# Optimization experiments

Measured on AMD Instinct MI355X. Metric: run time of the kernel, lower is better.

## Reference

```python
import jax, jax.numpy as jnp
import numpy as np

N, E = 50000, 800000
F_IN, F_EDGE = 64, 16
HEADS, C_HEAD = 4, 32
HC = HEADS * C_HEAD  # 128 = hidden_node_channels
MLP_IN = F_IN + HC   # 192
MLP0, MLP1 = 128, 128
NEG_SLOPE = 0.2


def leaky_relu(x):
    return jnp.where(x >= 0, x, NEG_SLOPE * x)


def layer_norm(x, g, b, eps=1e-5):
    mu = jnp.mean(x, axis=-1, keepdims=True)
    var = jnp.mean(jnp.square(x - mu), axis=-1, keepdims=True)
    return (x - mu) * jax.lax.rsqrt(var + eps) * g + b


def setup_inputs() -> dict:
    key = jax.random.key(0)
    ks = jax.random.split(key, 24)
    s = 0.05
    inp = {
        "node_features": jax.random.normal(ks[0], (N, F_IN), jnp.float32),
        "edge_features": jax.random.normal(ks[1], (E, F_EDGE), jnp.float32),
        "edge_index": jax.random.randint(ks[2], (2, E), 0, N, jnp.int32),
        # GATv2Conv params (share_weights=False, bias=True, edge_dim=16)
        "W_l": jax.random.normal(ks[3], (F_IN, HC), jnp.float32) * s,
        "b_l": jax.random.normal(ks[4], (HC,), jnp.float32) * s,
        "W_r": jax.random.normal(ks[5], (F_IN, HC), jnp.float32) * s,
        "b_r": jax.random.normal(ks[6], (HC,), jnp.float32) * s,
        "W_e": jax.random.normal(ks[7], (F_EDGE, HC), jnp.float32) * s,
        "att": jax.random.normal(ks[8], (HEADS, C_HEAD), jnp.float32) * s,
        "gat_bias": jax.random.normal(ks[9], (HC,), jnp.float32) * s,
        # residual_connection: Linear(64->128) + LayerNorm
        "res_W": jax.random.normal(ks[10], (F_IN, MLP1), jnp.float32) * s,
        "res_b": jax.random.normal(ks[11], (MLP1,), jnp.float32) * s,
        "res_g": 1.0 + jax.random.normal(ks[12], (MLP1,), jnp.float32) * s,
        "res_beta": jax.random.normal(ks[13], (MLP1,), jnp.float32) * s,
        # upd MLP: two ffn_blocks (Linear -> LayerNorm -> ReLU)
        "W0": jax.random.normal(ks[14], (MLP_IN, MLP0), jnp.float32) * s,
        "b0": jax.random.normal(ks[15], (MLP0,), jnp.float32) * s,
        "g0": 1.0 + jax.random.normal(ks[16], (MLP0,), jnp.float32) * s,
        "beta0": jax.random.normal(ks[17], (MLP0,), jnp.float32) * s,
        "W1": jax.random.normal(ks[18], (MLP0, MLP1), jnp.float32) * s,
        "b1": jax.random.normal(ks[19], (MLP1,), jnp.float32) * s,
        "g1": 1.0 + jax.random.normal(ks[20], (MLP1,), jnp.float32) * s,
        "beta1": jax.random.normal(ks[21], (MLP1,), jnp.float32) * s,
    }
    return inp


def reference(node_features, edge_features, edge_index,
              W_l, b_l, W_r, b_r, W_e, att, gat_bias,
              res_W, res_b, res_g, res_beta,
              W0, b0, g0, beta0, W1, b1, g1, beta1):
    src, dst = edge_index[0], edge_index[1]

    # ---- GATv2Conv ----
    x_l = (node_features @ W_l + b_l).reshape(N, HEADS, C_HEAD)  # source transform
    x_r = (node_features @ W_r + b_r).reshape(N, HEADS, C_HEAD)  # target transform
    e = (edge_features @ W_e).reshape(E, HEADS, C_HEAD)

    x_j = x_l[src]                      # [E,H,C] messages
    m = x_j + x_r[dst] + e              # [E,H,C]
    logits = jnp.sum(leaky_relu(m) * att, axis=-1)  # [E,H]

    # segment softmax over incoming edges of each destination node
    mx = jax.ops.segment_max(logits, dst, num_segments=N)      # [N,H]
    ex = jnp.exp(logits - mx[dst])                             # [E,H]
    den = jax.ops.segment_sum(ex, dst, num_segments=N)         # [N,H]
    alpha = ex / den[dst]                                      # [E,H]

    agg = jax.ops.segment_sum(alpha[..., None] * x_j, dst, num_segments=N)
    gat_out = agg.reshape(N, HC) + gat_bias                    # [N,128]

    # ---- residual concat-MLP ----
    identity = layer_norm(node_features @ res_W + res_b, res_g, res_beta)
    h = jnp.concatenate([node_features, gat_out], axis=-1)     # [N,192]
    h = jax.nn.relu(layer_norm(h @ W0 + b0, g0, beta0))
    h = jax.nn.relu(layer_norm(h @ W1 + b1, g1, beta1))
    return identity + h
```

## Files before the change

### kernel.cpp

```cpp
#include <hip/hip_runtime.h>

#define NN 50000
#define NE 800000
#define NB 196
#define K1B 782

typedef __attribute__((ext_vector_type(8))) short bf16x8;
typedef __attribute__((ext_vector_type(4))) float f32x4;
typedef __attribute__((ext_vector_type(2))) _Float16 h2f;

__device__ __forceinline__ int rfl(int v) { return __builtin_amdgcn_readfirstlane(v); }

__device__ __forceinline__ unsigned short bfb(float x) {
    union { float f; unsigned u; } v; v.f = x;
    unsigned r = v.u + 0x7FFFu + ((v.u >> 16) & 1u);
    return (unsigned short)(r >> 16);
}
__device__ __forceinline__ unsigned pkbf(float lo, float hi) {
    return ((unsigned)bfb(hi) << 16) | (unsigned)bfb(lo);
}
__device__ __forceinline__ float bf2f(unsigned short s) {
    union { unsigned u; float f; } v; v.u = ((unsigned)s) << 16; return v.f;
}
__device__ __forceinline__ unsigned pkh2(float a, float b) {
    union { h2f h; unsigned u; } x;
    x.h.x = (_Float16)a; x.h.y = (_Float16)b;
    return x.u;
}
__device__ __forceinline__ float fdot2u(unsigned a, unsigned b, float c) {
    union { unsigned u; h2f h; } ua, ub; ua.u = a; ub.u = b;
    return __builtin_amdgcn_fdot2(ua.h, ub.h, c, false);
}

__device__ __forceinline__ float dpp_reduce16(float p) {
    int t;
    t = __builtin_amdgcn_update_dpp(0, __float_as_int(p), 0xB1, 0xF, 0xF, false);
    p += __int_as_float(t);
    t = __builtin_amdgcn_update_dpp(0, __float_as_int(p), 0x4E, 0xF, 0xF, false);
    p += __int_as_float(t);
    t = __builtin_amdgcn_update_dpp(0, __float_as_int(p), 0x124, 0xF, 0xF, false);
    p += __int_as_float(t);
    t = __builtin_amdgcn_update_dpp(0, __float_as_int(p), 0x128, 0xF, 0xF, false);
    p += __int_as_float(t);
    return p;
}

__device__ __forceinline__ float exp2_hw(float x) {
    float r;
    asm("v_exp_f32 %0, %1" : "=v"(r) : "v"(x));
    return r;
}

__global__ __launch_bounds__(256) void k0_prep(
    const float* __restrict__ W_l, const float* __restrict__ W_r,
    const float* __restrict__ res_W, const float* __restrict__ W0,
    const float* __restrict__ W1, const float* __restrict__ W_e,
    unsigned short* __restrict__ Wtl, unsigned short* __restrict__ Wtr,
    unsigned short* __restrict__ Wtres, unsigned short* __restrict__ Wt0,
    unsigned short* __restrict__ Wt1,
    unsigned* __restrict__ Wep,
    int* __restrict__ deg, int* __restrict__ row_start)
{
    const int t0 = blockIdx.x * 256 + threadIdx.x;
    if (t0 < 24576) { int n = t0 / 192, k = t0 - n * 192; Wt0[t0] = bfb(W0[k * 128 + n]); }
    if (t0 < 16384) { int n = t0 >> 7, k = t0 & 127; Wt1[t0] = bfb(W1[k * 128 + n]); }
    if (t0 < 8192) {
        int n = t0 >> 6, k = t0 & 63;
        Wtl[t0]   = bfb(W_l[k * 128 + n]);
        Wtr[t0]   = bfb(W_r[k * 128 + n]);
        Wtres[t0] = bfb(res_W[k * 128 + n]);
    }
    if (t0 < 1024) {
        int c = t0 >> 3, j = t0 & 7;
        Wep[t0] = pkh2(W_e[(2 * j) * 128 + c], W_e[(2 * j + 1) * 128 + c]);
    }
    if (t0 < NN) deg[t0] = 0;
    if (t0 == 0) row_start[NN] = NE;
}

__global__ __launch_bounds__(256, 4) void ka_nodes_degree(
    const float* __restrict__ nf,
    const unsigned short* __restrict__ Wtl, const float* __restrict__ b_l,
    const unsigned short* __restrict__ Wtr, const float* __restrict__ b_r,
    const unsigned short* __restrict__ Wtres, const float* __restrict__ res_b,
    const float* __restrict__ res_g, const float* __restrict__ res_beta,
    unsigned* __restrict__ xlp, unsigned* __restrict__ xrp,
    unsigned* __restrict__ identp,
    const int* __restrict__ eidx, int* __restrict__ deg, int* __restrict__ rank,
    const float* __restrict__ ef, unsigned* __restrict__ efp)
{
    if (blockIdx.x >= K1B) {
        int e = (blockIdx.x - K1B) * 256 + threadIdx.x;
        if (e < NE) {
            rank[e] = atomicAdd(deg + eidx[NE + e], 1);
            const float4* er = (const float4*)(ef + (size_t)e * 16);
            float4 v0 = er[0], v1 = er[1], v2 = er[2], v3 = er[3];
            uint4 o0, o1;
            o0.x = pkh2(v0.x, v0.y); o0.y = pkh2(v0.z, v0.w);
            o0.z = pkh2(v1.x, v1.y); o0.w = pkh2(v1.z, v1.w);
            o1.x = pkh2(v2.x, v2.y); o1.y = pkh2(v2.z, v2.w);
            o1.z = pkh2(v3.x, v3.y); o1.w = pkh2(v3.z, v3.w);
            *(uint4*)(efp + (size_t)e * 8)     = o0;
            *(uint4*)(efp + (size_t)e * 8 + 4) = o1;
        }
        return;
    }
    __shared__ __align__(16) unsigned As32[64 * 36];
    const int tid = threadIdx.x;
    const int node0 = blockIdx.x * 64;

    for (int i = tid; i < 64 * 32; i += 256) {
        int n = i >> 5, c2 = i & 31;
        int gn = node0 + n;
        float2 v = make_float2(0.f, 0.f);
        if (gn < NN) v = *(const float2*)(nf + gn * 64 + 2 * c2);
        As32[n * 36 + c2] = pkbf(v.x, v.y);
    }
    __syncthreads();

    const int lane = tid & 63, w = tid >> 6;
    const int c = lane & 15, ko = lane >> 4;
    const unsigned short* As = (const unsigned short*)As32;
    bf16x8 a0 = *(const bf16x8*)(As + (w * 16 + c) * 72 + 0 * 32 + ko * 8);
    bf16x8 a1 = *(const bf16x8*)(As + (w * 16 + c) * 72 + 1 * 32 + ko * 8);
    const int lrow0 = node0 + w * 16 + 4 * ko;

    #pragma unroll
    for (int p = 0; p < 3; ++p) {
        const unsigned short* Wt = (p == 0) ? Wtl : (p == 1) ? Wtr : Wtres;
        f32x4 acc[8];
        #pragma unroll
        for (int nt = 0; nt < 8; ++nt) acc[nt] = f32x4{0.f, 0.f, 0.f, 0.f};
        #pragma unroll
        for (int nt = 0; nt < 8; ++nt) {
            bf16x8 bf0 = *(const bf16x8*)(Wt + (nt * 16 + c) * 64 + 0 * 32 + ko * 8);
            acc[nt] = __builtin_amdgcn_mfma_f32_16x16x32_bf16(a0, bf0, acc[nt], 0, 0, 0);
            bf16x8 bf1 = *(const bf16x8*)(Wt + (nt * 16 + c) * 64 + 1 * 32 + ko * 8);
            acc[nt] = __builtin_amdgcn_mfma_f32_16x16x32_bf16(a1, bf1, acc[nt], 0, 0, 0);
        }
        if (p < 2) {
            const float* bias = (p == 0) ? b_l : b_r;
            unsigned* outp = (p == 0) ? xlp : xrp;
            float bv[8];
            #pragma unroll
            for (int nt = 0; nt < 8; ++nt) bv[nt] = bias[nt * 16 + c];
            #pragma unroll
            for (int reg = 0; reg < 4; ++reg) {
                int row = lrow0 + reg;
                #pragma unroll
                for (int nt = 0; nt < 8; ++nt) {
                    float v = acc[nt][reg] + bv[nt];
                    float v2 = __shfl_xor(v, 1, 64);
                    if (row < NN && (lane & 1) == 0)
                        outp[row * 64 + nt * 8 + (c >> 1)] = pkh2(v, v2);
                }
            }
        } else {
            float bv[8], gv[8], tv[8];
            #pragma unroll
            for (int nt = 0; nt < 8; ++nt) {
                bv[nt] = res_b[nt * 16 + c];
                gv[nt] = res_g[nt * 16 + c];
                tv[nt] = res_beta[nt * 16 + c];
            }
            #pragma unroll
            for (int reg = 0; reg < 4; ++reg) {
                float sum = 0.f, sq = 0.f, hv[8];
                #pragma unroll
                for (int nt = 0; nt < 8; ++nt) {
                    float v = acc[nt][reg] + bv[nt];
                    hv[nt] = v; sum += v; sq += v * v;
                }
                #pragma unroll
                for (int m = 1; m <= 8; m <<= 1) {
                    sum += __shfl_xor(sum, m, 64);
                    sq  += __shfl_xor(sq, m, 64);
                }
                float mean = sum * (1.f / 128.f);
                float inv  = rsqrtf(sq * (1.f / 128.f) - mean * mean + 1e-5f);
                int row = lrow0 + reg;
                #pragma unroll
                for (int nt = 0; nt < 8; ++nt) {
                    float v = (hv[nt] - mean) * inv * gv[nt] + tv[nt];
                    float v2 = __shfl_xor(v, 1, 64);
                    if (row < NN && (lane & 1) == 0)
                        identp[row * 64 + nt * 8 + (c >> 1)] = pkbf(v, v2);
                }
            }
        }
    }
}

__global__ __launch_bounds__(256) void k3a_blocksum(
    const int* __restrict__ deg, int* __restrict__ bsum)
{
    __shared__ int ws[4];
    int i = blockIdx.x * 256 + threadIdx.x;
    int v = (i < NN) ? deg[i] : 0;
    #pragma unroll
    for (int m = 32; m >= 1; m >>= 1) v += __shfl_xor(v, m, 64);
    if ((threadIdx.x & 63) == 0) ws[threadIdx.x >> 6] = v;
    __syncthreads();
    if (threadIdx.x == 0) bsum[blockIdx.x] = ws[0] + ws[1] + ws[2] + ws[3];
}

__global__ __launch_bounds__(256) void k3c_apply(
    const int* __restrict__ deg, const int* __restrict__ bsum,
    int* __restrict__ row_start)
{
    __shared__ int wsum[4];
    __shared__ int roff[4];
    const int tid = threadIdx.x, lane = tid & 63, wid = tid >> 6;
    int bv = (tid < blockIdx.x) ? bsum[tid] : 0;
    #pragma unroll
    for (int m = 32; m >= 1; m >>= 1) bv += __shfl_xor(bv, m, 64);
    if (lane == 0) roff[wid] = bv;

    int i = blockIdx.x * 256 + tid;
    int v = (i < NN) ? deg[i] : 0;
    int sc = v;
    #pragma unroll
    for (int m = 1; m < 64; m <<= 1) {
        int t = __shfl_up(sc, m, 64);
        if (lane >= m) sc += t;
    }
    if (lane == 63) wsum[wid] = sc;
    __syncthreads();
    int off = roff[0] + roff[1] + roff[2] + roff[3];
    for (int w = 0; w < wid; ++w) off += wsum[w];
    int excl = off + sc - v;
    if (i < NN) row_start[i] = excl;
}

__global__ __launch_bounds__(256) void k4_scatter(
    const int* __restrict__ eidx, const int* __restrict__ row_start,
    const int* __restrict__ rank, int2* __restrict__ csr_es)
{
    int e = blockIdx.x * 256 + threadIdx.x;
    if (e >= NE) return;
    int dst = eidx[NE + e];
    csr_es[row_start[dst] + rank[e]] = make_int2(e, eidx[e]);
}

__global__ __launch_bounds__(256, 4) void k5_attn_aggregate(
    const int2* __restrict__ csr_es, const int* __restrict__ row_start,
    const unsigned* __restrict__ efp, const unsigned* __restrict__ Wep,
    const float* __restrict__ att,
    const unsigned* __restrict__ xlp, const unsigned* __restrict__ xrp,
    const float* __restrict__ gat_bias,
    unsigned* __restrict__ gatp)
{
    const int lane = threadIdx.x & 63;
    const int node = (blockIdx.x * 256 + threadIdx.x) >> 6;
    if (node >= NN) return;
    const int c = lane * 2;

    uint4 t0 = *(const uint4*)(Wep + c * 8);
    uint4 t1 = *(const uint4*)(Wep + c * 8 + 4);
    uint4 t2 = *(const uint4*)(Wep + (c + 1) * 8);
    uint4 t3 = *(const uint4*)(Wep + (c + 1) * 8 + 4);
    unsigned wx0 = t0.x, wx1 = t0.y, wx2 = t0.z, wx3 = t0.w;
    unsigned wx4 = t1.x, wx5 = t1.y, wx6 = t1.z, wx7 = t1.w;
    unsigned wy0 = t2.x, wy1 = t2.y, wy2 = t2.z, wy3 = t2.w;
    unsigned wy4 = t3.x, wy5 = t3.y, wy6 = t3.z, wy7 = t3.w;

    const float LOG2E = 1.44269504088896340736f;
    float2 a2 = *(const float2*)(att + c);
    a2.x *= LOG2E; a2.y *= LOG2E;
    float2 xr;
    {
        union { unsigned u; h2f h; } uxr;
        uxr.u = xrp[node * 64 + lane];
        xr.x = (float)uxr.h.x; xr.y = (float)uxr.h.y;
    }
    const uint4* __restrict__ efq = (const uint4*)efp;
    const unsigned* __restrict__ xlc = xlp + lane;

    const int sj  = rfl(row_start[node]);
    const int epj = rfl(row_start[node + 1]);

    float den = 0.f, n0 = 0.f, n1 = 0.f;

    for (int base = sj; base < epj; base += 64) {
        const int cnt = min(64, epj - base);
        const int2 mc = csr_es[base + lane];

        uint4 aE0, aE1, bE0, bE1, cE0, cE1, dE0, dE1, eE0, eE1, fE0, fE1;
        unsigned aX, bX, cX, dX, eX, fX;

#define LOADS(E0_, E1_, X_, K_)                                            \
        { int kk = (K_); if (kk >= cnt) kk = cnt - 1;                      \
          int eid  = __builtin_amdgcn_readlane(mc.x, kk);                  \
          int srcn = __builtin_amdgcn_readlane(mc.y, kk);                  \
          E0_ = efq[eid * 2 + 0]; E1_ = efq[eid * 2 + 1];                  \
          X_  = xlc[srcn * 64]; }

#define CONSUME(E0_, E1_, X_)                                              \
        { asm volatile("" : "+v"(wx0), "+v"(wx1), "+v"(wx2), "+v"(wx3),    \
                            "+v"(wx4), "+v"(wx5), "+v"(wx6), "+v"(wx7));   \
          asm volatile("" : "+v"(wy0), "+v"(wy1), "+v"(wy2), "+v"(wy3),    \
                            "+v"(wy4), "+v"(wy5), "+v"(wy6), "+v"(wy7));   \
          union { unsigned u; h2f h; } ux; ux.u = (X_);                    \
          float cx0 = (float)ux.h.x, cx1 = (float)ux.h.y;                  \
          float ax = cx0 + xr.x;                                           \
          float ay = cx1 + xr.y;                                           \
          float bx = 0.f, by = 0.f;                                        \
          ax = fdot2u((E0_).x, wx0, ax);  ay = fdot2u((E0_).x, wy0, ay);   \
          bx = fdot2u((E0_).y, wx1, bx);  by = fdot2u((E0_).y, wy1, by);   \
          ax = fdot2u((E0_).z, wx2, ax);  ay = fdot2u((E0_).z, wy2, ay);   \
          bx = fdot2u((E0_).w, wx3, bx);  by = fdot2u((E0_).w, wy3, by);   \
          ax = fdot2u((E1_).x, wx4, ax);  ay = fdot2u((E1_).x, wy4, ay);   \
          bx = fdot2u((E1_).y, wx5, bx);  by = fdot2u((E1_).y, wy5, by);   \
          ax = fdot2u((E1_).z, wx6, ax);  ay = fdot2u((E1_).z, wy6, ay);   \
          bx = fdot2u((E1_).w, wx7, bx);  by = fdot2u((E1_).w, wy7, by);   \
          float evx = ax + bx;                                             \
          float evy = ay + by;                                             \
          float lx = fmaxf(evx, 0.2f * evx);                               \
          float ly = fmaxf(evy, 0.2f * evy);                               \
          float p = lx * a2.x + ly * a2.y;                                 \
          p = dpp_reduce16(p);                                             \
          float ev = exp2_hw(p);                                           \
          den += ev; n0 += ev * cx0; n1 += ev * cx1; }

        LOADS(aE0, aE1, aX, 0);
        LOADS(bE0, bE1, bX, 1);
        LOADS(cE0, cE1, cX, 2);
        LOADS(dE0, dE1, dX, 3);
        LOADS(eE0, eE1, eX, 4);
        int j = 0;
        while (j + 6 <= cnt) {
            LOADS(fE0, fE1, fX, j + 5);
            CONSUME(aE0, aE1, aX);
            LOADS(aE0, aE1, aX, j + 6);
            CONSUME(bE0, bE1, bX);
            LOADS(bE0, bE1, bX, j + 7);
            CONSUME(cE0, cE1, cX);
            LOADS(cE0, cE1, cX, j + 8);
            CONSUME(dE0, dE1, dX);
            LOADS(dE0, dE1, dX, j + 9);
            CONSUME(eE0, eE1, eX);
            LOADS(eE0, eE1, eX, j + 10);
            CONSUME(fE0, fE1, fX);
            j += 6;
        }
        if (j < cnt)     CONSUME(aE0, aE1, aX);
        if (j + 1 < cnt) CONSUME(bE0, bE1, bX);
        if (j + 2 < cnt) CONSUME(cE0, cE1, cX);
        if (j + 3 < cnt) CONSUME(dE0, dE1, dX);
        if (j + 4 < cnt) CONSUME(eE0, eE1, eX);
#undef LOADS
#undef CONSUME
    }
    float rden = (den > 0.f) ? (1.f / den) : 0.f;
    float2 gb = *(const float2*)(gat_bias + c);
    float ox = n0 * rden + gb.x, oy = n1 * rden + gb.y;
    gatp[node * 64 + lane] = pkbf(ox, oy);
}

__global__ __launch_bounds__(256, 4) void k6_mlp_mfma(
    const float* __restrict__ nf, const unsigned* __restrict__ gatp,
    const unsigned* __restrict__ identp,
    const unsigned short* __restrict__ Wt0, const float* __restrict__ b0,
    const float* __restrict__ g0, const float* __restrict__ be0,
    const unsigned short* __restrict__ Wt1, const float* __restrict__ b1,
    const float* __restrict__ g1, const float* __restrict__ be1,
    float* __restrict__ out)
{
    __shared__ __align__(16) unsigned LDS[64 * 100];
    const int tid = threadIdx.x;
    const int node0 = blockIdx.x * 64;

    for (int i = tid; i < 64 * 96; i += 256) {
        int n = i / 96, c2 = i - n * 96;
        int gn = node0 + n;
        unsigned pv = 0u;
        if (gn < NN) {
            if (c2 < 32) {
                float2 v = *(const float2*)(nf + gn * 64 + 2 * c2);
                pv = pkbf(v.x, v.y);
            } else {
                pv = gatp[gn * 64 + (c2 - 32)];
            }
        }
        LDS[n * 100 + c2] = pv;
    }
    __syncthreads();

    const int lane = tid & 63, w = tid >> 6;
    const int c = lane & 15, ko = lane >> 4;
    const int lrow = w * 16 + 4 * ko;

    f32x4 acc[8];
    #pragma unroll
    for (int nt = 0; nt < 8; ++nt) acc[nt] = f32x4{0.f, 0.f, 0.f, 0.f};

    #pragma unroll
    for (int kb = 0; kb < 6; ++kb) {
        bf16x8 a = *(const bf16x8*)((const unsigned short*)LDS +
                                    (w * 16 + c) * 200 + kb * 32 + ko * 8);
        #pragma unroll
        for (int nt = 0; nt < 8; ++nt) {
            bf16x8 b = *(const bf16x8*)(Wt0 + (nt * 16 + c) * 192 + kb * 32 + ko * 8);
            acc[nt] = __builtin_amdgcn_mfma_f32_16x16x32_bf16(a, b, acc[nt], 0, 0, 0);
        }
    }

    float bv[8], gv[8], tv[8];
    #pragma unroll
    for (int nt = 0; nt < 8; ++nt) {
        bv[nt] = b0[nt * 16 + c];
        gv[nt] = g0[nt * 16 + c];
        tv[nt] = be0[nt * 16 + c];
    }
    __syncthreads();

    unsigned short* Hs = (unsigned short*)LDS;
    #pragma unroll
    for (int reg = 0; reg < 4; ++reg) {
        float sum = 0.f, sq = 0.f, hv[8];
        #pragma unroll
        for (int nt = 0; nt < 8; ++nt) {
            float v = acc[nt][reg] + bv[nt];
            hv[nt] = v; sum += v; sq += v * v;
        }
        #pragma unroll
        for (int m = 1; m <= 8; m <<= 1) {
            sum += __shfl_xor(sum, m, 64);
            sq  += __shfl_xor(sq, m, 64);
        }
        float mean = sum * (1.f / 128.f);
        float inv  = rsqrtf(sq * (1.f / 128.f) - mean * mean + 1e-5f);
        #pragma unroll
        for (int nt = 0; nt < 8; ++nt) {
            float h = fmaxf((hv[nt] - mean) * inv * gv[nt] + tv[nt], 0.f);
            Hs[(lrow + reg) * 136 + nt * 16 + c] = bfb(h);
        }
    }
    __syncthreads();

    #pragma unroll
    for (int nt = 0; nt < 8; ++nt) acc[nt] = f32x4{0.f, 0.f, 0.f, 0.f};
    #pragma unroll
    for (int kb = 0; kb < 4; ++kb) {
        bf16x8 a = *(const bf16x8*)((const unsigned short*)LDS +
                                    (w * 16 + c) * 136 + kb * 32 + ko * 8);
        #pragma unroll
        for (int nt = 0; nt < 8; ++nt) {
            bf16x8 b = *(const bf16x8*)(Wt1 + (nt * 16 + c) * 128 + kb * 32 + ko * 8);
            acc[nt] = __builtin_amdgcn_mfma_f32_16x16x32_bf16(a, b, acc[nt], 0, 0, 0);
        }
    }

    #pragma unroll
    for (int nt = 0; nt < 8; ++nt) {
        bv[nt] = b1[nt * 16 + c];
        gv[nt] = g1[nt * 16 + c];
        tv[nt] = be1[nt * 16 + c];
    }
    const int half = c & 1;
    #pragma unroll
    for (int reg = 0; reg < 4; ++reg) {
        float sum = 0.f, sq = 0.f, hv[8];
        #pragma unroll
        for (int nt = 0; nt < 8; ++nt) {
            float v = acc[nt][reg] + bv[nt];
            hv[nt] = v; sum += v; sq += v * v;
        }
        #pragma unroll
        for (int m = 1; m <= 8; m <<= 1) {
            sum += __shfl_xor(sum, m, 64);
            sq  += __shfl_xor(sq, m, 64);
        }
        float mean = sum * (1.f / 128.f);
        float inv  = rsqrtf(sq * (1.f / 128.f) - mean * mean + 1e-5f);
        int row = node0 + lrow + reg;
        if (row < NN) {
            #pragma unroll
            for (int nt = 0; nt < 8; ++nt) {
                float h = fmaxf((hv[nt] - mean) * inv * gv[nt] + tv[nt], 0.f);
                int col = nt * 16 + c;
                unsigned idw = identp[row * 64 + nt * 8 + (c >> 1)];
                float id = bf2f((unsigned short)(half ? (idw >> 16) : (idw & 0xFFFFu)));
                out[row * 128 + col] = id + h;
            }
        }
    }
}

extern "C" void kernel_launch(void* const* d_in, const int* in_sizes, int n_in,
                              void* d_out, int out_size, void* d_ws, size_t ws_size,
                              hipStream_t stream)
{
    const float* nf       = (const float*)d_in[0];
    const float* ef       = (const float*)d_in[1];
    const int*   eidx     = (const int*)d_in[2];
    const float* W_l      = (const float*)d_in[3];
    const float* b_l      = (const float*)d_in[4];
    const float* W_r      = (const float*)d_in[5];
    const float* b_r      = (const float*)d_in[6];
    const float* W_e      = (const float*)d_in[7];
    const float* att      = (const float*)d_in[8];
    const float* gat_bias = (const float*)d_in[9];
    const float* res_W    = (const float*)d_in[10];
    const float* res_b    = (const float*)d_in[11];
    const float* res_g    = (const float*)d_in[12];
    const float* res_beta = (const float*)d_in[13];
    const float* W0       = (const float*)d_in[14];
    const float* b0       = (const float*)d_in[15];
    const float* g0       = (const float*)d_in[16];
    const float* beta0    = (const float*)d_in[17];
    const float* W1       = (const float*)d_in[18];
    const float* b1       = (const float*)d_in[19];
    const float* g1       = (const float*)d_in[20];
    const float* beta1    = (const float*)d_in[21];
    float* out = (float*)d_out;

    char* ws = (char*)d_ws;
    size_t off = 0;
    auto alloc = [&](size_t bytes) -> void* {
        void* p = ws + off;
        off += (bytes + 255) & ~(size_t)255;
        return p;
    };
    unsigned* xlp    = (unsigned*)alloc((size_t)NN * 64 * 4);
    unsigned* xrp    = (unsigned*)alloc((size_t)NN * 64 * 4);
    unsigned* identp = (unsigned*)alloc((size_t)NN * 64 * 4);
    int* deg       = (int*)alloc((size_t)NN * 4);
    int* row_start = (int*)alloc((size_t)(NN + 1) * 4);
    int* rank      = (int*)alloc((size_t)NE * 4);
    int* bsum      = (int*)alloc((size_t)(NB + 1) * 4);
    int2* csr_es   = (int2*)alloc((size_t)(NE + 64) * 8);
    unsigned* gatp = (unsigned*)alloc((size_t)NN * 64 * 4);
    unsigned short* Wtl   = (unsigned short*)alloc(8192 * 2);
    unsigned short* Wtr   = (unsigned short*)alloc(8192 * 2);
    unsigned short* Wtres = (unsigned short*)alloc(8192 * 2);
    unsigned short* Wt0   = (unsigned short*)alloc(24576 * 2);
    unsigned short* Wt1   = (unsigned short*)alloc(16384 * 2);
    unsigned* Wep = (unsigned*)alloc(1024 * 4);
    unsigned* efp = (unsigned*)alloc((size_t)NE * 8 * 4);

    k0_prep<<<NB, 256, 0, stream>>>(W_l, W_r, res_W, W0, W1, W_e,
                                    Wtl, Wtr, Wtres, Wt0, Wt1, Wep,
                                    deg, row_start);

    ka_nodes_degree<<<K1B + (NE + 255) / 256, 256, 0, stream>>>(
        nf, Wtl, b_l, Wtr, b_r, Wtres, res_b, res_g, res_beta,
        xlp, xrp, identp, eidx, deg, rank, ef, efp);

    k3a_blocksum<<<NB, 256, 0, stream>>>(deg, bsum);
    k3c_apply<<<NB, 256, 0, stream>>>(deg, bsum, row_start);

    k4_scatter<<<(NE + 255) / 256, 256, 0, stream>>>(eidx, row_start, rank, csr_es);

    k5_attn_aggregate<<<(NN * 64 + 255) / 256, 256, 0, stream>>>(
        csr_es, row_start, efp, Wep, att, xlp, xrp, gat_bias, gatp);

    k6_mlp_mfma<<<(NN + 63) / 64, 256, 0, stream>>>(
        nf, gatp, identp, Wt0, b0, g0, beta0, Wt1, b1, g1, beta1, out);
}
```

Measured before the change: 332.7 us.

## Scatter packed edge features into CSR order for contiguous reads in attention

The fp16 packing of edge features moves from the degree kernel into the CSR scatter kernel, which now writes them directly at their sorted CSR position. The attention kernel then reads edge features contiguously per destination instead of gathering by edge id, and the CSR entry shrinks from an int2 to a single source index. The cost is 32-byte scattered writes in the scatter kernel in place of coalesced writes, while the gathered reads in the aggregation kernel become sequential.

```diff
diff --git a/kernel.cpp b/kernel.cpp
--- a/kernel.cpp
+++ b/kernel.cpp
@@ -86,23 +86,11 @@
     const float* __restrict__ res_g, const float* __restrict__ res_beta,
     unsigned* __restrict__ xlp, unsigned* __restrict__ xrp,
     unsigned* __restrict__ identp,
-    const int* __restrict__ eidx, int* __restrict__ deg, int* __restrict__ rank,
-    const float* __restrict__ ef, unsigned* __restrict__ efp)
+    const int* __restrict__ eidx, int* __restrict__ deg, int* __restrict__ rank)
 {
     if (blockIdx.x >= K1B) {
         int e = (blockIdx.x - K1B) * 256 + threadIdx.x;
-        if (e < NE) {
-            rank[e] = atomicAdd(deg + eidx[NE + e], 1);
-            const float4* er = (const float4*)(ef + (size_t)e * 16);
-            float4 v0 = er[0], v1 = er[1], v2 = er[2], v3 = er[3];
-            uint4 o0, o1;
-            o0.x = pkh2(v0.x, v0.y); o0.y = pkh2(v0.z, v0.w);
-            o0.z = pkh2(v1.x, v1.y); o0.w = pkh2(v1.z, v1.w);
-            o1.x = pkh2(v2.x, v2.y); o1.y = pkh2(v2.z, v2.w);
-            o1.z = pkh2(v3.x, v3.y); o1.w = pkh2(v3.z, v3.w);
-            *(uint4*)(efp + (size_t)e * 8)     = o0;
-            *(uint4*)(efp + (size_t)e * 8 + 4) = o1;
-        }
+        if (e < NE) rank[e] = atomicAdd(deg + eidx[NE + e], 1);
         return;
     }
     __shared__ __align__(16) unsigned As32[64 * 36];
@@ -234,17 +222,29 @@
 
 __global__ __launch_bounds__(256) void k4_scatter(
     const int* __restrict__ eidx, const int* __restrict__ row_start,
-    const int* __restrict__ rank, int2* __restrict__ csr_es)
+    const int* __restrict__ rank, const float* __restrict__ ef,
+    int* __restrict__ csr_src, unsigned* __restrict__ csr_ef)
 {
     int e = blockIdx.x * 256 + threadIdx.x;
     if (e >= NE) return;
     int dst = eidx[NE + e];
-    csr_es[row_start[dst] + rank[e]] = make_int2(e, eidx[e]);
+    int pos = row_start[dst] + rank[e];
+    csr_src[pos] = eidx[e];
+
+    const float4* er = (const float4*)(ef + (size_t)e * 16);
+    float4 v0 = er[0], v1 = er[1], v2 = er[2], v3 = er[3];
+    uint4 o0, o1;
+    o0.x = pkh2(v0.x, v0.y); o0.y = pkh2(v0.z, v0.w);
+    o0.z = pkh2(v1.x, v1.y); o0.w = pkh2(v1.z, v1.w);
+    o1.x = pkh2(v2.x, v2.y); o1.y = pkh2(v2.z, v2.w);
+    o1.z = pkh2(v3.x, v3.y); o1.w = pkh2(v3.z, v3.w);
+    *(uint4*)(csr_ef + (size_t)pos * 8)     = o0;
+    *(uint4*)(csr_ef + (size_t)pos * 8 + 4) = o1;
 }
 
 __global__ __launch_bounds__(256, 4) void k5_attn_aggregate(
-    const int2* __restrict__ csr_es, const int* __restrict__ row_start,
-    const unsigned* __restrict__ efp, const unsigned* __restrict__ Wep,
+    const int* __restrict__ csr_src, const int* __restrict__ row_start,
+    const unsigned* __restrict__ csr_ef, const unsigned* __restrict__ Wep,
     const float* __restrict__ att,
     const unsigned* __restrict__ xlp, const unsigned* __restrict__ xrp,
     const float* __restrict__ gat_bias,
@@ -273,7 +273,7 @@
         uxr.u = xrp[node * 64 + lane];
         xr.x = (float)uxr.h.x; xr.y = (float)uxr.h.y;
     }
-    const uint4* __restrict__ efq = (const uint4*)efp;
+    const uint4* __restrict__ cef = (const uint4*)csr_ef;
     const unsigned* __restrict__ xlc = xlp + lane;
 
     const int sj  = rfl(row_start[node]);
@@ -283,16 +283,16 @@
 
     for (int base = sj; base < epj; base += 64) {
         const int cnt = min(64, epj - base);
-        const int2 mc = csr_es[base + lane];
+        const int msrc = csr_src[base + lane];
 
         uint4 aE0, aE1, bE0, bE1, cE0, cE1, dE0, dE1, eE0, eE1, fE0, fE1;
         unsigned aX, bX, cX, dX, eX, fX;
 
 #define LOADS(E0_, E1_, X_, K_)                                            \
         { int kk = (K_); if (kk >= cnt) kk = cnt - 1;                      \
-          int eid  = __builtin_amdgcn_readlane(mc.x, kk);                  \
-          int srcn = __builtin_amdgcn_readlane(mc.y, kk);                  \
-          E0_ = efq[eid * 2 + 0]; E1_ = efq[eid * 2 + 1];                  \
+          int srcn = __builtin_amdgcn_readlane(msrc, kk);                  \
+          int ep = (base + kk) * 2;                                        \
+          E0_ = cef[ep]; E1_ = cef[ep + 1];                                \
           X_  = xlc[srcn * 64]; }
 
 #define CONSUME(E0_, E1_, X_)                                              \
@@ -529,7 +529,8 @@
     int* row_start = (int*)alloc((size_t)(NN + 1) * 4);
     int* rank      = (int*)alloc((size_t)NE * 4);
     int* bsum      = (int*)alloc((size_t)(NB + 1) * 4);
-    int2* csr_es   = (int2*)alloc((size_t)(NE + 64) * 8);
+    int* csr_src   = (int*)alloc((size_t)(NE + 64) * 4);
+    unsigned* csr_ef = (unsigned*)alloc((size_t)NE * 8 * 4);
     unsigned* gatp = (unsigned*)alloc((size_t)NN * 64 * 4);
     unsigned short* Wtl   = (unsigned short*)alloc(8192 * 2);
     unsigned short* Wtr   = (unsigned short*)alloc(8192 * 2);
@@ -537,7 +538,6 @@
     unsigned short* Wt0   = (unsigned short*)alloc(24576 * 2);
     unsigned short* Wt1   = (unsigned short*)alloc(16384 * 2);
     unsigned* Wep = (unsigned*)alloc(1024 * 4);
-    unsigned* efp = (unsigned*)alloc((size_t)NE * 8 * 4);
 
     k0_prep<<<NB, 256, 0, stream>>>(W_l, W_r, res_W, W0, W1, W_e,
                                     Wtl, Wtr, Wtres, Wt0, Wt1, Wep,
@@ -545,15 +545,16 @@
 
     ka_nodes_degree<<<K1B + (NE + 255) / 256, 256, 0, stream>>>(
         nf, Wtl, b_l, Wtr, b_r, Wtres, res_b, res_g, res_beta,
-        xlp, xrp, identp, eidx, deg, rank, ef, efp);
+        xlp, xrp, identp, eidx, deg, rank);
 
     k3a_blocksum<<<NB, 256, 0, stream>>>(deg, bsum);
     k3c_apply<<<NB, 256, 0, stream>>>(deg, bsum, row_start);
 
-    k4_scatter<<<(NE + 255) / 256, 256, 0, stream>>>(eidx, row_start, rank, csr_es);
+    k4_scatter<<<(NE + 255) / 256, 256, 0, stream>>>(
+        eidx, row_start, rank, ef, csr_src, csr_ef);
 
     k5_attn_aggregate<<<(NN * 64 + 255) / 256, 256, 0, stream>>>(
-        csr_es, row_start, efp, Wep, att, xlp, xrp, gat_bias, gatp);
+        csr_src, row_start, csr_ef, Wep, att, xlp, xrp, gat_bias, gatp);
 
     k6_mlp_mfma<<<(NN + 63) / 64, 256, 0, stream>>>(
         nf, gatp, identp, Wt0, b0, g0, beta0, Wt1, b1, g1, beta1, out);
```

After: 347.2 us. 1.04x slower.
